# Kernel tuning notes

Measured on AMD Instinct MI355X. Metric: run time of the kernel, lower is better.

Reference implementation:

```python
import jax, jax.numpy as jnp
import numpy as np

N_NODES = 50000
N_EDGES = 1600000
IN_CH = 128
OUT_CH = 16
K_HOPS = 2


def setup_inputs() -> dict:
    key = jax.random.key(0)
    k1, k2, k3, k4 = jax.random.split(key, 4)
    x = jax.random.normal(k1, (N_NODES, IN_CH), dtype=jnp.float32)
    W = jax.random.normal(k2, (OUT_CH, IN_CH), dtype=jnp.float32) * 0.05
    edge_weight = jax.random.uniform(k3, (N_EDGES,), dtype=jnp.float32)
    edge_index = jax.random.randint(k4, (2, N_EDGES), 0, N_NODES, dtype=jnp.int64)
    return {"x": x, "W": W, "edge_weight": edge_weight,
            "edge_index": edge_index, "K": K_HOPS}


def reference(x, W, edge_weight, edge_index, K):
    N = x.shape[0]
    # --- gcn_norm with add_self_loops=True (fill_value = 1.0) ---
    loops = jnp.arange(N, dtype=edge_index.dtype)
    row = jnp.concatenate([edge_index[0], loops])  # source nodes
    col = jnp.concatenate([edge_index[1], loops])  # target nodes
    w = jnp.concatenate([edge_weight, jnp.ones((N,), dtype=x.dtype)])
    deg = jax.ops.segment_sum(w, col, num_segments=N)  # degree at targets
    dinv = jnp.where(deg > 0, jax.lax.rsqrt(deg), 0.0)
    norm = dinv[row] * w * dinv[col]  # [E+N]

    # --- K-hop propagation: h <- A_hat @ h (gather-scale-scatter) ---
    def hop(h, _):
        msgs = norm[:, None] * h[row]               # [E+N, F] gather + scale
        h = jax.ops.segment_sum(msgs, col, num_segments=N)  # scatter-add
        return h, None

    h, _ = jax.lax.scan(hop, x, None, length=K)

    # --- linear projection (bias=False) then log_softmax over classes ---
    logits = h @ W.T  # [N, out_channels]
    return jax.nn.log_softmax(logits, axis=1)
```

## Files before the change

kernel.cpp:

```cpp
#include <hip/hip_runtime.h>
#include <math.h>

#define IN_CH 128
#define OUT_CH 16
#define B 256
#define CH_H 2048
#define CH_P 4096
#define LSH 6
#define LNODES 64
#define MAXNL 1024
#define MAXGH 2048

__device__ __forceinline__ void scan_nl(const unsigned* __restrict__ vals, unsigned* dst,
                                        unsigned* sums, int NL) {
    int tid = threadIdx.x;
    int b0 = tid * 4;
    unsigned v[4]; unsigned loc = 0;
#pragma unroll
    for (int q = 0; q < 4; ++q) { int i = b0 + q; v[q] = (i < NL) ? vals[i] : 0u; loc += v[q]; }
    sums[tid] = loc;
    __syncthreads();
    for (int off = 1; off < B; off <<= 1) {
        unsigned a = (tid >= off) ? sums[tid - off] : 0u;
        __syncthreads();
        sums[tid] += a;
        __syncthreads();
    }
    unsigned run = sums[tid] - loc;
#pragma unroll
    for (int q = 0; q < 4; ++q) { int i = b0 + q; if (i < NL) dst[i] = run; run += v[q]; }
    __syncthreads();
}

__global__ void __launch_bounds__(B) k_hist(const int* __restrict__ col,
                                            unsigned* __restrict__ bh, int E, int NL) {
    __shared__ unsigned hc[MAXNL];
    int tid = threadIdx.x;
    for (int i = tid; i < NL; i += B) hc[i] = 0u;
    __syncthreads();
    int base = blockIdx.x * CH_H;
    int end = base + CH_H < E ? base + CH_H : E;
    for (int e = base + tid; e < end; e += B)
        atomicAdd(&hc[col[e] >> LSH], 1u);
    __syncthreads();
    unsigned* out = bh + (size_t)blockIdx.x * NL;
    for (int i = tid; i < NL; i += B) out[i] = hc[i];
}

__global__ void __launch_bounds__(B) k_colscan(unsigned* __restrict__ bh,
                                               unsigned* __restrict__ tot, int G, int NL) {
    int j = blockIdx.x;
    __shared__ unsigned s[B];
    int tid = threadIdx.x;
    unsigned carry = 0;
    for (int g0 = 0; g0 < G; g0 += B) {
        __syncthreads();
        int g = g0 + tid;
        unsigned v = (g < G) ? bh[(size_t)g * NL + j] : 0u;
        s[tid] = v;
        __syncthreads();
        for (int off = 1; off < B; off <<= 1) {
            unsigned add = (tid >= off) ? s[tid - off] : 0u;
            __syncthreads();
            s[tid] += add;
            __syncthreads();
        }
        if (g < G) bh[(size_t)g * NL + j] = carry + s[tid] - v;
        carry += s[B - 1];
    }
    if (tid == 0) tot[j] = carry;
}

__global__ void __launch_bounds__(B)
k_place(const int* __restrict__ row, const int* __restrict__ col, const float* __restrict__ ew,
        const unsigned* __restrict__ bh, const unsigned* __restrict__ tot,
        uint2* __restrict__ rec, int E, int NL, int F) {
    __shared__ uint2 srec[CH_P];
    __shared__ unsigned short slf[CH_P];
    __shared__ unsigned gbase[MAXNL];
    __shared__ unsigned lscan[MAXNL];
    __shared__ unsigned lctr[MAXNL];
    __shared__ unsigned sums[B];
    int tid = threadIdx.x;
    int c = blockIdx.x;
    int base = c * CH_P;
    int end = base + CH_P < E ? base + CH_P : E;
    int cnt = end - base;

    scan_nl(tot, gbase, sums, NL);
    for (int i = tid; i < NL; i += B) lctr[i] = 0u;
    __syncthreads();
    for (int j = tid; j < cnt; j += B)
        atomicAdd(&lctr[col[base + j] >> LSH], 1u);
    __syncthreads();
    scan_nl(lctr, lscan, sums, NL);
    for (int i = tid; i < NL; i += B) lctr[i] = lscan[i];
    __syncthreads();
    for (int j = tid; j < cnt; j += B) {
        int e = base + j;
        int cc = col[e];
        int lf = cc >> LSH;
        unsigned pos = atomicAdd(&lctr[lf], 1u);
        srec[pos] = make_uint2(((unsigned)row[e] << 6) | (unsigned)(cc & (LNODES - 1)),
                               __float_as_uint(ew[e]));
        slf[pos] = (unsigned short)lf;
    }
    __syncthreads();
    const unsigned* myb = bh + (size_t)(c * F) * NL;
    for (int j = tid; j < cnt; j += B) {
        int lf = slf[j];
        unsigned outp = gbase[lf] + myb[lf] + ((unsigned)j - lscan[lf]);
        rec[outp] = srec[j];
    }
}

__global__ void __launch_bounds__(B)
k_sort2(const uint2* __restrict__ rec, const unsigned* __restrict__ tot,
        uint2* __restrict__ rec2, unsigned* __restrict__ nptr, int N, int NL) {
    __shared__ unsigned sums[B];
    __shared__ unsigned gbase[MAXNL];
    __shared__ unsigned hist[LNODES];
    __shared__ unsigned start[LNODES];
    int l = blockIdx.x, tid = threadIdx.x;
    scan_nl(tot, gbase, sums, NL);
    int seg = (int)gbase[l];
    int end = seg + (int)tot[l];
    if (tid < LNODES) hist[tid] = 0u;
    __syncthreads();
    for (int j = seg + tid; j < end; j += B)
        atomicAdd(&hist[rec[j].x & (LNODES - 1)], 1u);
    __syncthreads();
    if (tid < LNODES) {
        unsigned v = hist[tid];
        unsigned sum = v;
        for (int off = 1; off < LNODES; off <<= 1) {
            unsigned o = __shfl_up(sum, off, 64);
            if (tid >= off) sum += o;
        }
        unsigned st = (unsigned)seg + sum - v;
        start[tid] = st;
        int n = l * LNODES + tid;
        if (n < N) nptr[n] = st;
    }
    if (l == NL - 1 && tid == 0) nptr[N] = (unsigned)end;
    __syncthreads();
    for (int j = seg + tid; j < end; j += B) {
        uint2 u = rec[j];
        unsigned pos = atomicAdd(&start[u.x & (LNODES - 1)], 1u);
        rec2[pos] = make_uint2(u.x >> 6, u.y);
    }
}

__global__ void __launch_bounds__(B)
k_proj(const float* __restrict__ x, const float* __restrict__ W,
       const uint2* __restrict__ rec2, const unsigned* __restrict__ nptr,
       float* __restrict__ dinv, float* __restrict__ y, int N) {
    __shared__ float sW[OUT_CH * 132];
    int tid = threadIdx.x;
    for (int i = tid; i < OUT_CH * IN_CH; i += B) {
        int o = i >> 7, k = i & 127;
        sW[o * 132 + k] = W[i];
    }
    __syncthreads();
    int n = blockIdx.x * 16 + (tid >> 4);
    int o = tid & 15;
    if (n >= N) return;
    int j0 = (int)nptr[n], j1 = (int)nptr[n + 1];
    float wsum = 0.f;
    for (int j = j0 + o; j < j1; j += 16) wsum += __uint_as_float(rec2[j].y);
#pragma unroll
    for (int off = 1; off < 16; off <<= 1) wsum += __shfl_xor(wsum, off, 16);
    float dn = rsqrtf(1.0f + wsum);
    const float* xr = x + (size_t)n * IN_CH;
    const float* wr = sW + o * 132;
    float acc = 0.0f;
#pragma unroll
    for (int k = 0; k < IN_CH; k += 4) {
        float4 xv = *reinterpret_cast<const float4*>(xr + k);
        float4 wv = *reinterpret_cast<const float4*>(wr + k);
        acc += xv.x * wv.x + xv.y * wv.y + xv.z * wv.z + xv.w * wv.w;
    }
    y[(size_t)n * OUT_CH + o] = dn * acc;
    if (o == 0) dinv[n] = dn;
}

template <bool FINAL>
__global__ void __launch_bounds__(B)
k_hop(const uint2* __restrict__ rec2, const unsigned* __restrict__ nptr,
      const float* __restrict__ dinv, const float* __restrict__ gin,
      float* __restrict__ out, int N) {
    int t = blockIdx.x * B + threadIdx.x;
    int n = t >> 4, ch = t & 15;
    if (n >= N) return;
    int j0 = (int)nptr[n], j1 = (int)nptr[n + 1];
    float acc = 0.f;
    int j = j0;
    for (; j + 3 < j1; j += 4) {
        uint2 u0 = rec2[j], u1 = rec2[j + 1], u2 = rec2[j + 2], u3 = rec2[j + 3];
        acc += __uint_as_float(u0.y) * gin[(size_t)u0.x * OUT_CH + ch]
             + __uint_as_float(u1.y) * gin[(size_t)u1.x * OUT_CH + ch]
             + __uint_as_float(u2.y) * gin[(size_t)u2.x * OUT_CH + ch]
             + __uint_as_float(u3.y) * gin[(size_t)u3.x * OUT_CH + ch];
    }
    for (; j < j1; ++j) {
        uint2 u = rec2[j];
        acc += __uint_as_float(u.y) * gin[(size_t)u.x * OUT_CH + ch];
    }
    float d = dinv[n];
    float s = gin[(size_t)n * OUT_CH + ch] + acc;
    if (!FINAL) {
        out[(size_t)n * OUT_CH + ch] = d * d * s;
    } else {
        float v = d * s;
        float m = v;
#pragma unroll
        for (int off = 1; off < 16; off <<= 1) m = fmaxf(m, __shfl_xor(m, off, 16));
        float se = expf(v - m);
#pragma unroll
        for (int off = 1; off < 16; off <<= 1) se += __shfl_xor(se, off, 16);
        out[(size_t)n * OUT_CH + ch] = v - m - logf(se);
    }
}


__global__ void fb_deginit(float* deg, int N) {
    int i = blockIdx.x * blockDim.x + threadIdx.x;
    if (i < N) deg[i] = 1.0f;
}
__global__ void fb_deg(const int* __restrict__ col, const float* __restrict__ ew,
                       float* deg, int E) {
    int e = blockIdx.x * blockDim.x + threadIdx.x;
    if (e < E) atomicAdd(&deg[col[e]], ew[e]);
}
__global__ void fb_dinv(const float* __restrict__ deg, float* dinv, int N) {
    int i = blockIdx.x * blockDim.x + threadIdx.x;
    if (i < N) dinv[i] = rsqrtf(deg[i]);
}
__global__ void fb_proj(const float* __restrict__ x, const float* __restrict__ W,
                        float* __restrict__ y, int N) {
    __shared__ float sW[OUT_CH * 132];
    for (int i = threadIdx.x; i < OUT_CH * IN_CH; i += blockDim.x) {
        int o = i >> 7, k = i & 127;
        sW[o * 132 + k] = W[i];
    }
    __syncthreads();
    int t = threadIdx.x;
    int n = blockIdx.x * 16 + (t >> 4);
    int o = t & 15;
    if (n >= N) return;
    const float* xr = x + (size_t)n * IN_CH;
    const float* wr = sW + o * 132;
    float acc = 0.0f;
#pragma unroll
    for (int k = 0; k < IN_CH; k += 4) {
        float4 xv = *reinterpret_cast<const float4*>(xr + k);
        float4 wv = *reinterpret_cast<const float4*>(wr + k);
        acc += xv.x * wv.x + xv.y * wv.y + xv.z * wv.z + xv.w * wv.w;
    }
    y[(size_t)n * OUT_CH + o] = acc;
}
__global__ void fb_selfinit(const float* __restrict__ hin, const float* __restrict__ dinv,
                            float* __restrict__ hout, int N) {
    int idx = blockIdx.x * blockDim.x + threadIdx.x;
    if (idx < N * OUT_CH) {
        float d = dinv[idx >> 4];
        hout[idx] = d * d * hin[idx];
    }
}
__global__ void fb_scat(const int* __restrict__ row, const int* __restrict__ col,
                        const float* __restrict__ ew, const float* __restrict__ dinv,
                        const float* __restrict__ hin, float* __restrict__ hout, int E) {
    long long idx = (long long)blockIdx.x * blockDim.x + threadIdx.x;
    int e = (int)(idx >> 4);
    int c = (int)(idx & 15);
    if (e >= E) return;
    int r = row[e], cl = col[e];
    float nv = dinv[r] * ew[e] * dinv[cl];
    atomicAdd(&hout[(size_t)cl * OUT_CH + c], nv * hin[(size_t)r * OUT_CH + c]);
}
__global__ void fb_lsm(const float* __restrict__ h, float* __restrict__ out, int N) {
    int n = blockIdx.x * blockDim.x + threadIdx.x;
    if (n >= N) return;
    const float* hr = h + (size_t)n * OUT_CH;
    float v[OUT_CH];
#pragma unroll
    for (int i = 0; i < OUT_CH; i++) v[i] = hr[i];
    float m = v[0];
#pragma unroll
    for (int i = 1; i < OUT_CH; i++) m = fmaxf(m, v[i]);
    float s = 0.0f;
#pragma unroll
    for (int i = 0; i < OUT_CH; i++) s += expf(v[i] - m);
    float lse = m + logf(s);
    float* orow = out + (size_t)n * OUT_CH;
#pragma unroll
    for (int i = 0; i < OUT_CH; i++) orow[i] = v[i] - lse;
}


extern "C" void kernel_launch(void* const* d_in, const int* in_sizes, int n_in,
                              void* d_out, int out_size, void* d_ws, size_t ws_size,
                              hipStream_t stream) {
    const float* x  = (const float*)d_in[0];
    const float* W  = (const float*)d_in[1];
    const float* ew = (const float*)d_in[2];
    const int*   ei = (const int*)d_in[3];

    int N = in_sizes[0] / IN_CH;
    int E = in_sizes[2];
    const int* row = ei;
    const int* col = ei + E;

    auto al = [](size_t v) { return (v + 255) & ~(size_t)255; };
    size_t N16 = (size_t)N * OUT_CH;

    int NL  = (N + LNODES - 1) >> LSH;
    int G_H = (E + CH_H - 1) / CH_H;
    int G_P = (E + CH_P - 1) / CH_P;
    int F   = CH_P / CH_H;
    int gH  = (int)((N16 + B - 1) / B);

    size_t o_rec2 = 0;
    size_t o_rec  = o_rec2 + al((size_t)E * 8);
    size_t o_tot  = o_rec  + al((size_t)E * 8);
    size_t o_nptr = o_tot  + al((size_t)NL * 4);
    size_t o_dinv = o_nptr + al((size_t)(N + 1) * 4);
    size_t need   = o_dinv + al((size_t)N * 4);

    bool bh_fits = ((size_t)G_H * NL * 4 <= al((size_t)E * 8));
    bool g_fits  = (2 * al(N16 * 4) <= al((size_t)E * 8));
    bool shape_ok = (NL <= MAXNL && G_H <= MAXGH && N <= MAXNL * LNODES &&
                     (G_P * F) <= G_H + F);

    char* ws = (char*)d_ws;

    if (shape_ok && bh_fits && g_fits && need <= ws_size) {
        uint2*    rec2 = (uint2*)(ws + o_rec2);
        unsigned* bh   = (unsigned*)(ws + o_rec2);
        uint2*    rec  = (uint2*)(ws + o_rec);
        float*    g0   = (float*)(ws + o_rec);
        float*    g1   = (float*)(ws + o_rec + al(N16 * 4));
        unsigned* tot  = (unsigned*)(ws + o_tot);
        unsigned* nptr = (unsigned*)(ws + o_nptr);
        float*    dinv = (float*)(ws + o_dinv);

        k_hist   <<<G_H, B, 0, stream>>>(col, bh, E, NL);
        k_colscan<<<NL,  B, 0, stream>>>(bh, tot, G_H, NL);
        k_place  <<<G_P, B, 0, stream>>>(row, col, ew, bh, tot, rec, E, NL, F);
        k_sort2  <<<NL,  B, 0, stream>>>(rec, tot, rec2, nptr, N, NL);
        k_proj   <<<(N + 15) / 16, B, 0, stream>>>(x, W, rec2, nptr, dinv, g0, N);
        k_hop<false><<<gH, B, 0, stream>>>(rec2, nptr, dinv, g0, g1, N);
        k_hop<true ><<<gH, B, 0, stream>>>(rec2, nptr, dinv, g1, (float*)d_out, N);
    } else {
        size_t f_deg  = 0;
        size_t f_dinv = f_deg  + al((size_t)N * 4);
        size_t f_h0   = f_dinv + al((size_t)N * 4);
        size_t f_h1   = f_h0   + al(N16 * 4);
        float* deg  = (float*)(ws + f_deg);
        float* dinv = (float*)(ws + f_dinv);
        float* h0   = (float*)(ws + f_h0);
        float* h1   = (float*)(ws + f_h1);

        int gN   = (N + B - 1) / B;
        int gE   = (E + B - 1) / B;
        int gN16 = (N * OUT_CH + B - 1) / B;
        long long scat = (long long)E * OUT_CH;
        int gScat = (int)((scat + B - 1) / B);

        fb_deginit<<<gN, B, 0, stream>>>(deg, N);
        fb_deg<<<gE, B, 0, stream>>>(col, ew, deg, E);
        fb_dinv<<<gN, B, 0, stream>>>(deg, dinv, N);
        fb_proj<<<(N + 15) / 16, B, 0, stream>>>(x, W, h0, N);
        float* hin = h0; float* hout = h1;
        for (int k = 0; k < 2; k++) {
            fb_selfinit<<<gN16, B, 0, stream>>>(hin, dinv, hout, N);
            fb_scat<<<gScat, B, 0, stream>>>(row, col, ew, dinv, hin, hout, E);
            float* t = hin; hin = hout; hout = t;
        }
        fb_lsm<<<gN, B, 0, stream>>>(hin, (float*)d_out, N);
    }
}
```

Measured before the change: 128.3 us.

## Fuse degree and projection into sort kernel, pack CSR records to 32-bit

Merges the projection kernel into the per-bucket sort kernel: degree sums are accumulated with shared-memory float atomics during the histogram pass, and the x@W^T projection runs for the block's 64 nodes. CSR records are packed into 32 bits (16-bit source index, fp16 edge weight), halving edge traffic in both hop kernels. The workspace layout is reorganised so buffers no longer alias. This drops one launch and one pass over the records, but fp16 weights lose precision, the node count is capped at 65536, and the projection now runs on only NL blocks.

```diff
diff --git a/kernel.cpp b/kernel.cpp
--- a/kernel.cpp
+++ b/kernel.cpp
@@ -1,4 +1,5 @@
 #include <hip/hip_runtime.h>
+#include <hip/hip_fp16.h>
 #include <math.h>
 
 #define IN_CH 128
@@ -10,6 +11,18 @@
 #define LNODES 64
 #define MAXNL 1024
 #define MAXGH 2048
+
+__device__ __forceinline__ unsigned short f2h(float f) {
+    __half h = __float2half(f);
+    unsigned short u;
+    __builtin_memcpy(&u, &h, 2);
+    return u;
+}
+__device__ __forceinline__ float h2f(unsigned short u) {
+    __half h;
+    __builtin_memcpy(&h, &u, 2);
+    return __half2float(h);
+}
 
 __device__ __forceinline__ void scan_nl(const unsigned* __restrict__ vals, unsigned* dst,
                                         unsigned* sums, int NL) {
@@ -115,20 +128,34 @@
 }
 
 __global__ void __launch_bounds__(B)
-k_sort2(const uint2* __restrict__ rec, const unsigned* __restrict__ tot,
-        uint2* __restrict__ rec2, unsigned* __restrict__ nptr, int N, int NL) {
+k_sort2proj(const uint2* __restrict__ rec, const unsigned* __restrict__ tot,
+            const float* __restrict__ x, const float* __restrict__ W,
+            unsigned* __restrict__ rec2, unsigned* __restrict__ nptr,
+            float* __restrict__ dinv, float* __restrict__ g0, int N, int NL) {
     __shared__ unsigned sums[B];
     __shared__ unsigned gbase[MAXNL];
     __shared__ unsigned hist[LNODES];
     __shared__ unsigned start[LNODES];
+    __shared__ float dacc[LNODES];
+    __shared__ float dloc[LNODES];
+    __shared__ float sW[OUT_CH * 132];
     int l = blockIdx.x, tid = threadIdx.x;
+
+    for (int i = tid; i < OUT_CH * IN_CH; i += B) {
+        int o = i >> 7, k = i & 127;
+        sW[o * 132 + k] = W[i];
+    }
     scan_nl(tot, gbase, sums, NL);
     int seg = (int)gbase[l];
     int end = seg + (int)tot[l];
-    if (tid < LNODES) hist[tid] = 0u;
-    __syncthreads();
-    for (int j = seg + tid; j < end; j += B)
-        atomicAdd(&hist[rec[j].x & (LNODES - 1)], 1u);
+    if (tid < LNODES) { hist[tid] = 0u; dacc[tid] = 0.f; }
+    __syncthreads();
+    for (int j = seg + tid; j < end; j += B) {
+        uint2 u = rec[j];
+        int cc = (int)(u.x & (LNODES - 1));
+        atomicAdd(&hist[cc], 1u);
+        atomicAdd(&dacc[cc], __uint_as_float(u.y));
+    }
     __syncthreads();
     if (tid < LNODES) {
         unsigned v = hist[tid];
@@ -139,54 +166,39 @@
         }
         unsigned st = (unsigned)seg + sum - v;
         start[tid] = st;
+        float dn = rsqrtf(1.0f + dacc[tid]);
+        dloc[tid] = dn;
         int n = l * LNODES + tid;
-        if (n < N) nptr[n] = st;
+        if (n < N) { nptr[n] = st; dinv[n] = dn; }
     }
     if (l == NL - 1 && tid == 0) nptr[N] = (unsigned)end;
     __syncthreads();
     for (int j = seg + tid; j < end; j += B) {
         uint2 u = rec[j];
-        unsigned pos = atomicAdd(&start[u.x & (LNODES - 1)], 1u);
-        rec2[pos] = make_uint2(u.x >> 6, u.y);
-    }
-}
-
-__global__ void __launch_bounds__(B)
-k_proj(const float* __restrict__ x, const float* __restrict__ W,
-       const uint2* __restrict__ rec2, const unsigned* __restrict__ nptr,
-       float* __restrict__ dinv, float* __restrict__ y, int N) {
-    __shared__ float sW[OUT_CH * 132];
-    int tid = threadIdx.x;
-    for (int i = tid; i < OUT_CH * IN_CH; i += B) {
-        int o = i >> 7, k = i & 127;
-        sW[o * 132 + k] = W[i];
-    }
-    __syncthreads();
-    int n = blockIdx.x * 16 + (tid >> 4);
+        int cc = (int)(u.x & (LNODES - 1));
+        unsigned pos = atomicAdd(&start[cc], 1u);
+        rec2[pos] = ((u.x >> 6) << 16) | (unsigned)f2h(__uint_as_float(u.y));
+    }
     int o = tid & 15;
-    if (n >= N) return;
-    int j0 = (int)nptr[n], j1 = (int)nptr[n + 1];
-    float wsum = 0.f;
-    for (int j = j0 + o; j < j1; j += 16) wsum += __uint_as_float(rec2[j].y);
-#pragma unroll
-    for (int off = 1; off < 16; off <<= 1) wsum += __shfl_xor(wsum, off, 16);
-    float dn = rsqrtf(1.0f + wsum);
-    const float* xr = x + (size_t)n * IN_CH;
-    const float* wr = sW + o * 132;
-    float acc = 0.0f;
-#pragma unroll
-    for (int k = 0; k < IN_CH; k += 4) {
-        float4 xv = *reinterpret_cast<const float4*>(xr + k);
-        float4 wv = *reinterpret_cast<const float4*>(wr + k);
-        acc += xv.x * wv.x + xv.y * wv.y + xv.z * wv.z + xv.w * wv.w;
-    }
-    y[(size_t)n * OUT_CH + o] = dn * acc;
-    if (o == 0) dinv[n] = dn;
+    for (int nl = tid >> 4; nl < LNODES; nl += 16) {
+        int n = l * LNODES + nl;
+        if (n >= N) break;
+        const float* xr = x + (size_t)n * IN_CH;
+        const float* wr = sW + o * 132;
+        float acc = 0.0f;
+#pragma unroll
+        for (int k = 0; k < IN_CH; k += 4) {
+            float4 xv = *reinterpret_cast<const float4*>(xr + k);
+            float4 wv = *reinterpret_cast<const float4*>(wr + k);
+            acc += xv.x * wv.x + xv.y * wv.y + xv.z * wv.z + xv.w * wv.w;
+        }
+        g0[(size_t)n * OUT_CH + o] = dloc[nl] * acc;
+    }
 }
 
 template <bool FINAL>
 __global__ void __launch_bounds__(B)
-k_hop(const uint2* __restrict__ rec2, const unsigned* __restrict__ nptr,
+k_hop(const unsigned* __restrict__ rec2, const unsigned* __restrict__ nptr,
       const float* __restrict__ dinv, const float* __restrict__ gin,
       float* __restrict__ out, int N) {
     int t = blockIdx.x * B + threadIdx.x;
@@ -196,15 +208,15 @@
     float acc = 0.f;
     int j = j0;
     for (; j + 3 < j1; j += 4) {
-        uint2 u0 = rec2[j], u1 = rec2[j + 1], u2 = rec2[j + 2], u3 = rec2[j + 3];
-        acc += __uint_as_float(u0.y) * gin[(size_t)u0.x * OUT_CH + ch]
-             + __uint_as_float(u1.y) * gin[(size_t)u1.x * OUT_CH + ch]
-             + __uint_as_float(u2.y) * gin[(size_t)u2.x * OUT_CH + ch]
-             + __uint_as_float(u3.y) * gin[(size_t)u3.x * OUT_CH + ch];
+        unsigned u0 = rec2[j], u1 = rec2[j + 1], u2 = rec2[j + 2], u3 = rec2[j + 3];
+        acc += h2f((unsigned short)u0) * gin[(size_t)(u0 >> 16) * OUT_CH + ch]
+             + h2f((unsigned short)u1) * gin[(size_t)(u1 >> 16) * OUT_CH + ch]
+             + h2f((unsigned short)u2) * gin[(size_t)(u2 >> 16) * OUT_CH + ch]
+             + h2f((unsigned short)u3) * gin[(size_t)(u3 >> 16) * OUT_CH + ch];
     }
     for (; j < j1; ++j) {
-        uint2 u = rec2[j];
-        acc += __uint_as_float(u.y) * gin[(size_t)u.x * OUT_CH + ch];
+        unsigned u = rec2[j];
+        acc += h2f((unsigned short)u) * gin[(size_t)(u >> 16) * OUT_CH + ch];
     }
     float d = dinv[n];
     float s = gin[(size_t)n * OUT_CH + ch] + acc;
@@ -320,35 +332,35 @@
     int F   = CH_P / CH_H;
     int gH  = (int)((N16 + B - 1) / B);
 
-    size_t o_rec2 = 0;
-    size_t o_rec  = o_rec2 + al((size_t)E * 8);
-    size_t o_tot  = o_rec  + al((size_t)E * 8);
+    size_t o_rec  = 0;
+    size_t o_rec2 = o_rec  + al((size_t)E * 8);
+    size_t o_bh   = o_rec2 + al((size_t)E * 4);
+    size_t o_tot  = o_bh   + al((size_t)G_H * NL * 4);
     size_t o_nptr = o_tot  + al((size_t)NL * 4);
     size_t o_dinv = o_nptr + al((size_t)(N + 1) * 4);
-    size_t need   = o_dinv + al((size_t)N * 4);
-
-    bool bh_fits = ((size_t)G_H * NL * 4 <= al((size_t)E * 8));
-    bool g_fits  = (2 * al(N16 * 4) <= al((size_t)E * 8));
-    bool shape_ok = (NL <= MAXNL && G_H <= MAXGH && N <= MAXNL * LNODES &&
+    size_t o_g0   = o_dinv + al((size_t)N * 4);
+    size_t o_g1   = o_g0   + al(N16 * 4);
+    size_t need   = o_g1   + al(N16 * 4);
+
+    bool shape_ok = (NL <= MAXNL && G_H <= MAXGH && N <= 65536 &&
                      (G_P * F) <= G_H + F);
 
     char* ws = (char*)d_ws;
 
-    if (shape_ok && bh_fits && g_fits && need <= ws_size) {
-        uint2*    rec2 = (uint2*)(ws + o_rec2);
-        unsigned* bh   = (unsigned*)(ws + o_rec2);
+    if (shape_ok && need <= ws_size) {
         uint2*    rec  = (uint2*)(ws + o_rec);
-        float*    g0   = (float*)(ws + o_rec);
-        float*    g1   = (float*)(ws + o_rec + al(N16 * 4));
+        unsigned* rec2 = (unsigned*)(ws + o_rec2);
+        unsigned* bh   = (unsigned*)(ws + o_bh);
         unsigned* tot  = (unsigned*)(ws + o_tot);
         unsigned* nptr = (unsigned*)(ws + o_nptr);
         float*    dinv = (float*)(ws + o_dinv);
-
-        k_hist   <<<G_H, B, 0, stream>>>(col, bh, E, NL);
-        k_colscan<<<NL,  B, 0, stream>>>(bh, tot, G_H, NL);
-        k_place  <<<G_P, B, 0, stream>>>(row, col, ew, bh, tot, rec, E, NL, F);
-        k_sort2  <<<NL,  B, 0, stream>>>(rec, tot, rec2, nptr, N, NL);
-        k_proj   <<<(N + 15) / 16, B, 0, stream>>>(x, W, rec2, nptr, dinv, g0, N);
+        float*    g0   = (float*)(ws + o_g0);
+        float*    g1   = (float*)(ws + o_g1);
+
+        k_hist     <<<G_H, B, 0, stream>>>(col, bh, E, NL);
+        k_colscan  <<<NL,  B, 0, stream>>>(bh, tot, G_H, NL);
+        k_place    <<<G_P, B, 0, stream>>>(row, col, ew, bh, tot, rec, E, NL, F);
+        k_sort2proj<<<NL,  B, 0, stream>>>(rec, tot, x, W, rec2, nptr, dinv, g0, N, NL);
         k_hop<false><<<gH, B, 0, stream>>>(rec2, nptr, dinv, g0, g1, N);
         k_hop<true ><<<gH, B, 0, stream>>>(rec2, nptr, dinv, g1, (float*)d_out, N);
     } else {
```

Measured after the change: 124.4 us. 3.0% less time.
